# Kernel optimization log

Measured on AMD Instinct MI355X. Metric: run time of the kernel, lower is better.

The kernel has to match this reference:

```python
import jax, jax.numpy as jnp
import numpy as np

V, D, H, L, FF, BS = 50257, 1024, 16, 8, 4096, 1024
B, T = 2, 1024
HD = D // H
SCALE = 1.0 / np.sqrt(HD)
STD = 0.02


def setup_inputs() -> dict:
    key = jax.random.key(0)
    ks = jax.random.split(key, 8)
    rn = lambda k, s: (jax.random.normal(k, s, jnp.float32) * STD)
    return {
        'idx': jax.random.randint(ks[0], (B, T), 0, V),
        'tok_emb': rn(ks[1], (V, D)),
        'pos_emb': rn(ks[2], (1, BS, D)),
        'ln1_w': jnp.ones((L, D)), 'ln1_b': jnp.zeros((L, D)),
        'qkv_w': rn(ks[3], (L, 3 * D, D)), 'qkv_b': jnp.zeros((L, 3 * D)),
        'proj_w': rn(ks[4], (L, D, D)), 'proj_b': jnp.zeros((L, D)),
        'ln2_w': jnp.ones((L, D)), 'ln2_b': jnp.zeros((L, D)),
        'fc1_w': rn(ks[5], (L, FF, D)), 'fc1_b': jnp.zeros((L, FF)),
        'fc2_w': rn(ks[6], (L, D, FF)), 'fc2_b': jnp.zeros((L, D)),
        'lnf_w': jnp.ones((D,)), 'lnf_b': jnp.zeros((D,)),
    }


def layernorm(x, w, b, eps=1e-5):
    mu = jnp.mean(x, axis=-1, keepdims=True)
    var = jnp.mean(jnp.square(x - mu), axis=-1, keepdims=True)
    return (x - mu) * jax.lax.rsqrt(var + eps) * w + b


def _forward(idx, tok_emb, pos_emb, ln1_w, ln1_b, qkv_w, qkv_b, proj_w, proj_b,
             ln2_w, ln2_b, fc1_w, fc1_b, fc2_w, fc2_b, lnf_w, lnf_b):
    b, t = idx.shape
    x = tok_emb[idx] + pos_emb[0, :t]           # [B,T,D]; dropout identity in eval
    mask = jnp.tril(jnp.ones((t, t), dtype=bool))  # causal

    def block(x, p):
        l1w, l1b, qw, qb, pw, pb, l2w, l2b, f1w, f1b, f2w, f2b = p
        h = layernorm(x, l1w, l1b)
        qkv = h @ qw.T + qb                      # [B,T,3D]
        qkv = qkv.reshape(b, t, 3, H, HD)
        q, k, v = qkv[:, :, 0], qkv[:, :, 1], qkv[:, :, 2]  # [B,T,H,HD]
        att = jnp.einsum('bqhd,bkhd->bhqk', q, k) * SCALE
        att = jnp.where(mask, att, -jnp.inf)
        att = jax.nn.softmax(att, axis=-1)       # attn dropout identity in eval
        y = jnp.einsum('bhqk,bkhd->bqhd', att, v).reshape(b, t, D)
        x = x + (y @ pw.T + pb)
        h = layernorm(x, l2w, l2b)
        h = jax.nn.gelu(h @ f1w.T + f1b, approximate=False)  # exact GELU as nn.GELU
        x = x + (h @ f2w.T + f2b)
        return x, None

    params = (ln1_w, ln1_b, qkv_w, qkv_b, proj_w, proj_b,
              ln2_w, ln2_b, fc1_w, fc1_b, fc2_w, fc2_b)
    x, _ = jax.lax.scan(block, x, params)
    x = layernorm(x, lnf_w, lnf_b)
    logits = x @ tok_emb.T                       # weight-tied head
    return logits


def reference(idx, tok_emb, pos_emb, ln1_w, ln1_b, qkv_w, qkv_b, proj_w, proj_b,
              ln2_w, ln2_b, fc1_w, fc1_b, fc2_w, fc2_b, lnf_w, lnf_b):
    return _forward(idx, tok_emb, pos_emb, ln1_w, ln1_b, qkv_w, qkv_b, proj_w,
                    proj_b, ln2_w, ln2_b, fc1_w, fc1_b, fc2_w, fc2_b, lnf_w, lnf_b)
```

## Files before the change

### kernel.cpp

```cpp
#include <hip/hip_runtime.h>
#include <cstdint>

#define Dm 1024
#define Tm 1024
#define Bm 2
#define Lm 8
#define FFm 4096
#define Vm 50257
#define Mm (Bm * Tm)
#define VPAD2 50432

typedef __bf16 bf16x8 __attribute__((ext_vector_type(8)));
typedef float f32x4 __attribute__((ext_vector_type(4)));
typedef unsigned short u16;
typedef unsigned int u32;
typedef u16 u16x8 __attribute__((ext_vector_type(8)));
typedef u16 u16x4 __attribute__((ext_vector_type(4)));

__device__ __forceinline__ u16 f2bf(float f) {
  u32 u = __float_as_uint(f);
  u += 0x7FFFu + ((u >> 16) & 1u);
  return (u16)(u >> 16);
}
__device__ __forceinline__ float bf2f(u16 u) {
  return __uint_as_float((u32)u << 16);
}
__device__ __forceinline__ u32 packbf(float lo, float hi) {
  return (u32)f2bf(lo) | ((u32)f2bf(hi) << 16);
}

__device__ __forceinline__ void gload16(const u16* g, u16* l) {
  __builtin_amdgcn_global_load_lds(
      (const __attribute__((address_space(1))) void*)g,
      (__attribute__((address_space(3))) void*)l, 16, 0, 0);
}

__global__ __launch_bounds__(256) void embed_k(
    const int* __restrict__ idx, const float* __restrict__ tok,
    const float* __restrict__ pos, float* __restrict__ x) {
  int m = blockIdx.x, t = threadIdx.x;
  int id = idx[m];
  int tt = m & (Tm - 1);
  float4 a = *(const float4*)(tok + (size_t)id * Dm + t * 4);
  float4 p = *(const float4*)(pos + (size_t)tt * Dm + t * 4);
  float4 o;
  o.x = a.x + p.x; o.y = a.y + p.y; o.z = a.z + p.z; o.w = a.w + p.w;
  *(float4*)(x + (size_t)m * Dm + t * 4) = o;
}

__global__ __launch_bounds__(256) void conv_k(const float* __restrict__ s,
                                              u16* __restrict__ d,
                                              long long nsrc, long long ntot) {
  long long i = ((long long)blockIdx.x * 256 + threadIdx.x) * 8;
  if (i >= ntot) return;
  u16x8 r = {0, 0, 0, 0, 0, 0, 0, 0};
  if (i < nsrc) {
    float4 a = *(const float4*)(s + i);
    float4 b = *(const float4*)(s + i + 4);
    r[0] = f2bf(a.x); r[1] = f2bf(a.y); r[2] = f2bf(a.z); r[3] = f2bf(a.w);
    r[4] = f2bf(b.x); r[5] = f2bf(b.y); r[6] = f2bf(b.z); r[7] = f2bf(b.w);
  }
  *(u16x8*)(d + i) = r;
}

#define R0 (3 * Dm * Dm)
#define R1 (Dm * Dm)
#define R2 (FFm * Dm)
#define R3 (Dm * FFm)
__global__ __launch_bounds__(256) void convw_k(
    const float* __restrict__ s0, const float* __restrict__ s1,
    const float* __restrict__ s2, const float* __restrict__ s3,
    u16* __restrict__ d) {
  size_t i = ((size_t)blockIdx.x * 256 + threadIdx.x) * 8;
  const float* s;
  size_t o;
  if (i < R0) { s = s0; o = i; }
  else if (i < (size_t)R0 + R1) { s = s1; o = i - R0; }
  else if (i < (size_t)R0 + R1 + R2) { s = s2; o = i - R0 - R1; }
  else { s = s3; o = i - R0 - R1 - R2; }
  float4 a = *(const float4*)(s + o);
  float4 b = *(const float4*)(s + o + 4);
  u16x8 r;
  r[0] = f2bf(a.x); r[1] = f2bf(a.y); r[2] = f2bf(a.z); r[3] = f2bf(a.w);
  r[4] = f2bf(b.x); r[5] = f2bf(b.y); r[6] = f2bf(b.z); r[7] = f2bf(b.w);
  *(u16x8*)(d + i) = r;
}

__global__ __launch_bounds__(256) void ln_k(const float* __restrict__ x,
                                            const float* __restrict__ w,
                                            const float* __restrict__ b,
                                            u16* __restrict__ out) {
  __shared__ float red[4];
  int row = blockIdx.x, t = threadIdx.x;
  float4 v = *(const float4*)(x + (size_t)row * Dm + t * 4);
  float s = v.x + v.y + v.z + v.w;
#pragma unroll
  for (int mm = 1; mm < 64; mm <<= 1) s += __shfl_xor(s, mm);
  if ((t & 63) == 0) red[t >> 6] = s;
  __syncthreads();
  float mu = (red[0] + red[1] + red[2] + red[3]) * (1.0f / Dm);
  __syncthreads();
  float dx = v.x - mu, dy = v.y - mu, dz = v.z - mu, dw = v.w - mu;
  float sq = dx * dx + dy * dy + dz * dz + dw * dw;
#pragma unroll
  for (int mm = 1; mm < 64; mm <<= 1) sq += __shfl_xor(sq, mm);
  if ((t & 63) == 0) red[t >> 6] = sq;
  __syncthreads();
  float var = (red[0] + red[1] + red[2] + red[3]) * (1.0f / Dm);
  float rs = rsqrtf(var + 1e-5f);
  float4 wv = *(const float4*)(w + t * 4);
  float4 bv = *(const float4*)(b + t * 4);
  u16x4 o;
  o[0] = f2bf(dx * rs * wv.x + bv.x);
  o[1] = f2bf(dy * rs * wv.y + bv.y);
  o[2] = f2bf(dz * rs * wv.z + bv.z);
  o[3] = f2bf(dw * rs * wv.w + bv.w);
  *(u16x4*)(out + (size_t)row * Dm + t * 4) = o;
}

__global__ __launch_bounds__(512, 2) void gemm8_k(
    const u16* __restrict__ A, const u16* __restrict__ W,
    const float* __restrict__ bias, float* __restrict__ Cf,
    u16* __restrict__ Cb, int ldc, int nstore, int K, int gelu, int mblks,
    int nblks) {
  __shared__ __align__(16) u16 As[4][8192];
  __shared__ __align__(16) u16 Ws[4][8192];
  int nwg = mblks * nblks;
  int orig = blockIdx.x;
  int q8 = nwg >> 3, r8 = nwg & 7, xcd = orig & 7, loc = orig >> 3;
  int wg = (xcd < r8 ? xcd * (q8 + 1) : r8 * (q8 + 1) + (xcd - r8) * q8) + loc;
  int bx = wg % mblks, by = wg / mblks;
  int m0 = bx << 8, n0 = by << 8;
  int t = threadIdx.x, wave = t >> 6, lane = t & 63;
  int wr = wave >> 2, wc = wave & 3;
  int lr = lane & 15, cq = lane >> 4;
  int sw8 = (cq ^ ((lr >> 1) & 3)) << 3;
  int row0 = t >> 2;
  int kcG = (t & 3) ^ ((t >> 3) & 3);
  const u16* gA = A + (size_t)(m0 + row0) * K + kcG * 8;
  const u16* gW = W + (size_t)(n0 + row0) * K + kcG * 8;
  size_t rstep = (size_t)128 * K;

  f32x4 acc[8][4] = {};
  int nch = K >> 5;

  for (int s = 0; s < 3; ++s) {
    gload16(gA + s * 32, &As[s][wave * 512]);
    gload16(gA + rstep + s * 32, &As[s][4096 + wave * 512]);
    gload16(gW + s * 32, &Ws[s][wave * 512]);
    gload16(gW + rstep + s * 32, &Ws[s][4096 + wave * 512]);
  }
  asm volatile("s_waitcnt vmcnt(8)");
  __builtin_amdgcn_s_barrier();

  for (int c = 0; c < nch; ++c) {
    const u16* sA = As[c & 3];
    const u16* sW = Ws[c & 3];
    bf16x8 afA[4], bfr[4], afB[4];
#pragma unroll
    for (int mi = 0; mi < 4; ++mi)
      afA[mi] = *(const bf16x8*)&sA[(wr * 128 + mi * 16 + lr) * 32 + sw8];
#pragma unroll
    for (int ni = 0; ni < 4; ++ni)
      bfr[ni] = *(const bf16x8*)&sW[(wc * 64 + ni * 16 + lr) * 32 + sw8];
#pragma unroll
    for (int mi = 0; mi < 4; ++mi)
      afB[mi] =
          *(const bf16x8*)&sA[(wr * 128 + (mi + 4) * 16 + lr) * 32 + sw8];
    if (c + 3 < nch) {
      int s3 = (c + 3) & 3;
      gload16(gA + (size_t)(c + 3) * 32, &As[s3][wave * 512]);
      gload16(gA + rstep + (size_t)(c + 3) * 32, &As[s3][4096 + wave * 512]);
    }
    __builtin_amdgcn_s_barrier();
    asm volatile("s_waitcnt lgkmcnt(4)");
    __builtin_amdgcn_s_setprio(1);
#pragma unroll
    for (int mi = 0; mi < 4; ++mi)
#pragma unroll
      for (int ni = 0; ni < 4; ++ni)
        acc[mi][ni] = __builtin_amdgcn_mfma_f32_16x16x32_bf16(
            afA[mi], bfr[ni], acc[mi][ni], 0, 0, 0);
    __builtin_amdgcn_s_setprio(0);
    __builtin_amdgcn_s_barrier();
    if (c + 3 < nch) {
      int s3 = (c + 3) & 3;
      gload16(gW + (size_t)(c + 3) * 32, &Ws[s3][wave * 512]);
      gload16(gW + rstep + (size_t)(c + 3) * 32, &Ws[s3][4096 + wave * 512]);
    }
    asm volatile("s_waitcnt lgkmcnt(0)");
    __builtin_amdgcn_s_setprio(1);
#pragma unroll
    for (int mi = 0; mi < 4; ++mi)
#pragma unroll
      for (int ni = 0; ni < 4; ++ni)
        acc[mi + 4][ni] = __builtin_amdgcn_mfma_f32_16x16x32_bf16(
            afB[mi], bfr[ni], acc[mi + 4][ni], 0, 0, 0);
    __builtin_amdgcn_s_setprio(0);
    if (c + 1 < nch) {
      if (c + 3 < nch)
        asm volatile("s_waitcnt vmcnt(8)");
      else if (c + 2 < nch)
        asm volatile("s_waitcnt vmcnt(4)");
      else
        asm volatile("s_waitcnt vmcnt(0)");
    }
    __builtin_amdgcn_s_barrier();
  }

  int gm0 = m0 + wr * 128 + (cq << 2);
  int gn0 = n0 + wc * 64 + lr;
#pragma unroll
  for (int mi = 0; mi < 8; ++mi) {
#pragma unroll
    for (int ni = 0; ni < 4; ++ni) {
      int gm = gm0 + mi * 16;
      int gn = gn0 + ni * 16;
      if (gn < nstore) {
        float bv = bias ? bias[gn] : 0.f;
#pragma unroll
        for (int j = 0; j < 4; ++j) {
          float o = acc[mi][ni][j] + bv;
          if (gelu) o = 0.5f * o * (1.0f + erff(o * 0.70710678118654752f));
          if (Cb) Cb[(size_t)(gm + j) * ldc + gn] = f2bf(o);
          else Cf[(size_t)(gm + j) * ldc + gn] = o;
        }
      }
    }
  }
}

__global__ __launch_bounds__(512, 2) void gemm8h_k(
    const u16* __restrict__ A, const u16* __restrict__ W,
    const float* __restrict__ bias, float* __restrict__ Cf,
    u16* __restrict__ Cb, int ldc, int nstore, int K, int gelu, int mblks,
    int nblks) {
  __shared__ __align__(16) u16 As[4][4096];
  __shared__ __align__(16) u16 Ws[4][8192];
  int nwg = mblks * nblks;
  int orig = blockIdx.x;
  int q8 = nwg >> 3, r8 = nwg & 7, xcd = orig & 7, loc = orig >> 3;
  int wg = (xcd < r8 ? xcd * (q8 + 1) : r8 * (q8 + 1) + (xcd - r8) * q8) + loc;
  int bx = wg % mblks, by = wg / mblks;
  int m0 = bx << 7, n0 = by << 8;
  int t = threadIdx.x, wave = t >> 6, lane = t & 63;
  int wr = wave >> 2, wc = wave & 3;
  int lr = lane & 15, cq = lane >> 4;
  int sw8 = (cq ^ ((lr >> 1) & 3)) << 3;
  int row0 = t >> 2;
  int kcG = (t & 3) ^ ((t >> 3) & 3);
  const u16* gA = A + (size_t)(m0 + row0) * K + kcG * 8;
  const u16* gW = W + (size_t)(n0 + row0) * K + kcG * 8;
  size_t rstep = (size_t)128 * K;

  f32x4 acc[4][4] = {};
  int nch = K >> 5;

  for (int s = 0; s < 3; ++s) {
    gload16(gA + s * 32, &As[s][wave * 512]);
    gload16(gW + s * 32, &Ws[s][wave * 512]);
    gload16(gW + rstep + s * 32, &Ws[s][4096 + wave * 512]);
  }
  asm volatile("s_waitcnt vmcnt(6)");
  __builtin_amdgcn_s_barrier();

  for (int c = 0; c < nch; ++c) {
    const u16* sA = As[c & 3];
    const u16* sW = Ws[c & 3];
    bf16x8 af[4], bf[4];
#pragma unroll
    for (int mi = 0; mi < 4; ++mi)
      af[mi] = *(const bf16x8*)&sA[(wr * 64 + mi * 16 + lr) * 32 + sw8];
#pragma unroll
    for (int ni = 0; ni < 4; ++ni)
      bf[ni] = *(const bf16x8*)&sW[(wc * 64 + ni * 16 + lr) * 32 + sw8];
    if (c + 3 < nch) {
      int s3 = (c + 3) & 3;
      gload16(gA + (size_t)(c + 3) * 32, &As[s3][wave * 512]);
      gload16(gW + (size_t)(c + 3) * 32, &Ws[s3][wave * 512]);
      gload16(gW + rstep + (size_t)(c + 3) * 32, &Ws[s3][4096 + wave * 512]);
    }
    __builtin_amdgcn_s_barrier();
    asm volatile("s_waitcnt lgkmcnt(0)");
    __builtin_amdgcn_s_setprio(1);
#pragma unroll
    for (int mi = 0; mi < 4; ++mi)
#pragma unroll
      for (int ni = 0; ni < 4; ++ni)
        acc[mi][ni] = __builtin_amdgcn_mfma_f32_16x16x32_bf16(
            af[mi], bf[ni], acc[mi][ni], 0, 0, 0);
    __builtin_amdgcn_s_setprio(0);
    if (c + 1 < nch) {
      if (c + 3 < nch)
        asm volatile("s_waitcnt vmcnt(6)");
      else if (c + 2 < nch)
        asm volatile("s_waitcnt vmcnt(3)");
      else
        asm volatile("s_waitcnt vmcnt(0)");
    }
    __builtin_amdgcn_s_barrier();
  }

  int gm0 = m0 + wr * 64 + (cq << 2);
  int gn0 = n0 + wc * 64 + lr;
#pragma unroll
  for (int mi = 0; mi < 4; ++mi) {
#pragma unroll
    for (int ni = 0; ni < 4; ++ni) {
      int gm = gm0 + mi * 16;
      int gn = gn0 + ni * 16;
      if (gn < nstore) {
        float bv = bias ? bias[gn] : 0.f;
#pragma unroll
        for (int j = 0; j < 4; ++j) {
          float o = acc[mi][ni][j] + bv;
          if (gelu) o = 0.5f * o * (1.0f + erff(o * 0.70710678118654752f));
          if (Cb) Cb[(size_t)(gm + j) * ldc + gn] = f2bf(o);
          else Cf[(size_t)(gm + j) * ldc + gn] = o;
        }
      }
    }
  }
}

__global__ __launch_bounds__(256) void gemm_k(
    const u16* __restrict__ A, const u16* __restrict__ W,
    const float* __restrict__ bias, const float* __restrict__ res,
    float* __restrict__ Cf, u16* __restrict__ Cb, int ldc, int nstore, int K,
    int gelu, int mblks, int nblks) {
  __shared__ __align__(16) u16 As[2][4096];
  __shared__ __align__(16) u16 Ws[2][4096];
  int id = blockIdx.x;
  int c = id & 7, m2 = id >> 3;
  int bx = m2 % mblks;
  int by = (m2 / mblks) * 8 + c;
  if (by >= nblks) return;
  int m0 = bx << 7, n0 = by << 7;
  int t = threadIdx.x;
  int wave = t >> 6, lane = t & 63;
  int wm = (wave & 1) << 6, wn = (wave >> 1) << 6;
  int lr = lane & 15, cq = lane >> 4;

  f32x4 acc[4][4] = {};

  int ch0 = wave * 64 + lane;
  int ch1 = 256 + ch0;
  int r0 = ch0 >> 2, c0 = (ch0 & 3) ^ ((r0 >> 1) & 3);
  int r1 = ch1 >> 2, c1 = (ch1 & 3) ^ ((r1 >> 1) & 3);
  const u16* gA0 = A + (size_t)(m0 + r0) * K + c0 * 8;
  const u16* gA1 = A + (size_t)(m0 + r1) * K + c1 * 8;
  const u16* gW0 = W + (size_t)(n0 + r0) * K + c0 * 8;
  const u16* gW1 = W + (size_t)(n0 + r1) * K + c1 * 8;

  int nst = K >> 5;
  gload16(gA0, &As[0][wave * 512]);
  gload16(gA1, &As[0][2048 + wave * 512]);
  gload16(gW0, &Ws[0][wave * 512]);
  gload16(gW1, &Ws[0][2048 + wave * 512]);
  __syncthreads();

  for (int i = 0; i < nst; ++i) {
    int cur = i & 1;
    if (i + 1 < nst) {
      int ko = (i + 1) << 5;
      gload16(gA0 + ko, &As[cur ^ 1][wave * 512]);
      gload16(gA1 + ko, &As[cur ^ 1][2048 + wave * 512]);
      gload16(gW0 + ko, &Ws[cur ^ 1][wave * 512]);
      gload16(gW1 + ko, &Ws[cur ^ 1][2048 + wave * 512]);
    }
    bf16x8 af[4], bf[4];
#pragma unroll
    for (int mi = 0; mi < 4; ++mi) {
      int rr = wm + mi * 16 + lr;
      af[mi] =
          *(const bf16x8*)&As[cur][rr * 32 + ((cq ^ ((rr >> 1) & 3)) << 3)];
    }
#pragma unroll
    for (int ni = 0; ni < 4; ++ni) {
      int rr = wn + ni * 16 + lr;
      bf[ni] =
          *(const bf16x8*)&Ws[cur][rr * 32 + ((cq ^ ((rr >> 1) & 3)) << 3)];
    }
#pragma unroll
    for (int mi = 0; mi < 4; ++mi)
#pragma unroll
      for (int ni = 0; ni < 4; ++ni)
        acc[mi][ni] = __builtin_amdgcn_mfma_f32_16x16x32_bf16(
            af[mi], bf[ni], acc[mi][ni], 0, 0, 0);
    __syncthreads();
  }

  int orow = cq << 2, ocol = lr;
#pragma unroll
  for (int mi = 0; mi < 4; ++mi) {
#pragma unroll
    for (int ni = 0; ni < 4; ++ni) {
      int gm = m0 + wm + mi * 16 + orow;
      int gn = n0 + wn + ni * 16 + ocol;
      if (gn < nstore) {
        float bv = bias ? bias[gn] : 0.f;
#pragma unroll
        for (int j = 0; j < 4; ++j) {
          float o = acc[mi][ni][j] + bv;
          if (gelu) o = 0.5f * o * (1.0f + erff(o * 0.70710678118654752f));
          if (res) o += res[(size_t)(gm + j) * ldc + gn];
          if (Cb) Cb[(size_t)(gm + j) * ldc + gn] = f2bf(o);
          else Cf[(size_t)(gm + j) * ldc + gn] = o;
        }
      }
    }
  }
}

__global__ __launch_bounds__(256) void gemmsk_k(
    const u16* __restrict__ A, const u16* __restrict__ W,
    const float* __restrict__ bias, float* __restrict__ C, int ldc, int K,
    int klen, int mblks, int nblks) {
  __shared__ __align__(16) u16 As[2][4096];
  __shared__ __align__(16) u16 Ws[2][4096];
  int id = blockIdx.x;
  int bx = id % mblks;
  int tmp = id / mblks;
  int by = tmp % nblks;
  int ks = tmp / nblks;
  int m0 = bx << 7, n0 = by << 7;
  int koff = ks * klen;
  int t = threadIdx.x;
  int wave = t >> 6, lane = t & 63;
  int wm = (wave & 1) << 6, wn = (wave >> 1) << 6;
  int lr = lane & 15, cq = lane >> 4;

  f32x4 acc[4][4] = {};

  int ch0 = wave * 64 + lane;
  int ch1 = 256 + ch0;
  int r0 = ch0 >> 2, c0 = (ch0 & 3) ^ ((r0 >> 1) & 3);
  int r1 = ch1 >> 2, c1 = (ch1 & 3) ^ ((r1 >> 1) & 3);
  const u16* gA0 = A + (size_t)(m0 + r0) * K + koff + c0 * 8;
  const u16* gA1 = A + (size_t)(m0 + r1) * K + koff + c1 * 8;
  const u16* gW0 = W + (size_t)(n0 + r0) * K + koff + c0 * 8;
  const u16* gW1 = W + (size_t)(n0 + r1) * K + koff + c1 * 8;

  int nst = klen >> 5;
  gload16(gA0, &As[0][wave * 512]);
  gload16(gA1, &As[0][2048 + wave * 512]);
  gload16(gW0, &Ws[0][wave * 512]);
  gload16(gW1, &Ws[0][2048 + wave * 512]);
  __syncthreads();

  for (int i = 0; i < nst; ++i) {
    int cur = i & 1;
    if (i + 1 < nst) {
      int ko = (i + 1) << 5;
      gload16(gA0 + ko, &As[cur ^ 1][wave * 512]);
      gload16(gA1 + ko, &As[cur ^ 1][2048 + wave * 512]);
      gload16(gW0 + ko, &Ws[cur ^ 1][wave * 512]);
      gload16(gW1 + ko, &Ws[cur ^ 1][2048 + wave * 512]);
    }
    bf16x8 af[4], bf[4];
#pragma unroll
    for (int mi = 0; mi < 4; ++mi) {
      int rr = wm + mi * 16 + lr;
      af[mi] =
          *(const bf16x8*)&As[cur][rr * 32 + ((cq ^ ((rr >> 1) & 3)) << 3)];
    }
#pragma unroll
    for (int ni = 0; ni < 4; ++ni) {
      int rr = wn + ni * 16 + lr;
      bf[ni] =
          *(const bf16x8*)&Ws[cur][rr * 32 + ((cq ^ ((rr >> 1) & 3)) << 3)];
    }
#pragma unroll
    for (int mi = 0; mi < 4; ++mi)
#pragma unroll
      for (int ni = 0; ni < 4; ++ni)
        acc[mi][ni] = __builtin_amdgcn_mfma_f32_16x16x32_bf16(
            af[mi], bf[ni], acc[mi][ni], 0, 0, 0);
    __syncthreads();
  }

  int orow = cq << 2, ocol = lr;
#pragma unroll
  for (int mi = 0; mi < 4; ++mi) {
#pragma unroll
    for (int ni = 0; ni < 4; ++ni) {
      int gm = m0 + wm + mi * 16 + orow;
      int gn = n0 + wn + ni * 16 + ocol;
      float bv = (ks == 0) ? bias[gn] : 0.f;
#pragma unroll
      for (int j = 0; j < 4; ++j)
        atomicAdd(&C[(size_t)(gm + j) * ldc + gn], acc[mi][ni][j] + bv);
    }
  }
}

__global__ __launch_bounds__(256) void vtr_k(const u16* __restrict__ qkv,
                                             u16* __restrict__ vt) {
  __shared__ u16 T[64 * 68];
  int bh = blockIdx.y;
  int b = bh >> 4, h = bh & 15;
  int t0 = blockIdx.x << 6;
  int tid = threadIdx.x;
  int r = tid >> 2, q4 = tid & 3;
  const u16* src = qkv + (size_t)(b * Tm + t0 + r) * 3072 + 2048 + h * 64 +
                   q4 * 16;
  *(u16x8*)&T[r * 68 + q4 * 16] = *(const u16x8*)src;
  *(u16x8*)&T[r * 68 + q4 * 16 + 8] = *(const u16x8*)(src + 8);
  __syncthreads();
  int dr = tid >> 2, kq = tid & 3;
  u16x8 o0, o1;
#pragma unroll
  for (int u = 0; u < 8; ++u) o0[u] = T[(kq * 16 + u) * 68 + dr];
#pragma unroll
  for (int u = 0; u < 8; ++u) o1[u] = T[(kq * 16 + 8 + u) * 68 + dr];
  u16* dst = vt + ((size_t)bh * 64 + dr) * 1024 + t0 + kq * 16;
  *(u16x8*)dst = o0;
  *(u16x8*)(dst + 8) = o1;
}

__global__ __launch_bounds__(256) void attn_k(const u16* __restrict__ qkv,
                                              const u16* __restrict__ vt,
                                              u16* __restrict__ y) {
  __shared__ __align__(16) u16 Ks[2][4096];
  __shared__ __align__(16) u16 Vs[2][4096];
  int qt = gridDim.x - 1 - blockIdx.x;
  int q0 = qt << 6;
  int bh = blockIdx.y;
  int b = bh >> 4, h = bh & 15;
  int t = threadIdx.x, wave = t >> 6, lane = t & 63;
  int lr = lane & 15, cq = lane >> 4;

  bf16x8 qf[2];
  {
    size_t base = (size_t)(b * Tm + q0 + wave * 16 + lr) * 3072 + h * 64;
#pragma unroll
    for (int ks = 0; ks < 2; ++ks) {
      u16x8 qa = *(const u16x8*)(qkv + base + ks * 32 + cq * 8);
#pragma unroll
      for (int u = 0; u < 8; ++u) qa[u] = f2bf(bf2f(qa[u]) * 0.125f);
      qf[ks] = *(bf16x8*)&qa;
    }
  }

  f32x4 accO[4] = {};
  float m_run = -1e30f, l_run = 0.f;

  int ch0 = wave * 64 + lane, ch1 = 256 + ch0;
  int kr0 = ch0 >> 3, kc0 = ((ch0 & 7) ^ (kr0 & 7)) << 3;
  int kr1 = ch1 >> 3, kc1 = ((ch1 & 7) ^ (kr1 & 7)) << 3;
  const u16* kbase = qkv + (size_t)b * Tm * 3072 + 1024 + h * 64;
  const u16* vbase = vt + (size_t)bh * 64 * 1024;

  {
    gload16(kbase + (size_t)kr0 * 3072 + kc0, &Ks[0][wave * 512]);
    gload16(kbase + (size_t)kr1 * 3072 + kc1, &Ks[0][2048 + wave * 512]);
    gload16(vbase + (size_t)kr0 * 1024 + kc0, &Vs[0][wave * 512]);
    gload16(vbase + (size_t)kr1 * 1024 + kc1, &Vs[0][2048 + wave * 512]);
  }
  __syncthreads();

  for (int tk = 0; tk <= qt; ++tk) {
    int cur = tk & 1;
    if (tk < qt) {
      int kb0 = (tk + 1) << 6;
      gload16(kbase + (size_t)(kb0 + kr0) * 3072 + kc0,
              &Ks[cur ^ 1][wave * 512]);
      gload16(kbase + (size_t)(kb0 + kr1) * 3072 + kc1,
              &Ks[cur ^ 1][2048 + wave * 512]);
      gload16(vbase + (size_t)kr0 * 1024 + kb0 + kc0,
              &Vs[cur ^ 1][wave * 512]);
      gload16(vbase + (size_t)kr1 * 1024 + kb0 + kc1,
              &Vs[cur ^ 1][2048 + wave * 512]);
    }

    f32x4 s[4] = {};
    __builtin_amdgcn_s_setprio(1);
#pragma unroll
    for (int ks = 0; ks < 2; ++ks)
#pragma unroll
      for (int ni = 0; ni < 4; ++ni) {
        int rk = ni * 16 + lr;
        int ck = ks * 4 + cq;
        bf16x8 kf = *(const bf16x8*)&Ks[cur][rk * 64 + ((ck ^ (rk & 7)) << 3)];
        s[ni] = __builtin_amdgcn_mfma_f32_16x16x32_bf16(kf, qf[ks], s[ni],
                                                        0, 0, 0);
      }
    __builtin_amdgcn_s_setprio(0);

    if (tk == qt) {
      int kb0 = tk << 6;
      int qa = q0 + wave * 16 + lr;
#pragma unroll
      for (int ni = 0; ni < 4; ++ni)
#pragma unroll
        for (int r = 0; r < 4; ++r)
          if (kb0 + ni * 16 + cq * 4 + r > qa) s[ni][r] = -1e30f;
    }

    float mx = fmaxf(fmaxf(s[0][0], s[0][1]), fmaxf(s[0][2], s[0][3]));
#pragma unroll
    for (int ni = 1; ni < 4; ++ni)
      mx = fmaxf(mx, fmaxf(fmaxf(s[ni][0], s[ni][1]),
                           fmaxf(s[ni][2], s[ni][3])));
    mx = fmaxf(mx, __shfl_xor(mx, 16));
    mx = fmaxf(mx, __shfl_xor(mx, 32));
    float mn = fmaxf(m_run, mx);
    float alpha = __expf(m_run - mn);
    m_run = mn;
    float ls = 0.f;
    u32 packed[4][2];
#pragma unroll
    for (int ni = 0; ni < 4; ++ni) {
      float p0 = __expf(s[ni][0] - mn), p1 = __expf(s[ni][1] - mn);
      float p2 = __expf(s[ni][2] - mn), p3 = __expf(s[ni][3] - mn);
      ls += (p0 + p1) + (p2 + p3);
      packed[ni][0] = packbf(p0, p1);
      packed[ni][1] = packbf(p2, p3);
    }
    ls += __shfl_xor(ls, 16);
    ls += __shfl_xor(ls, 32);
    l_run = l_run * alpha + ls;

#pragma unroll
    for (int j = 0; j < 4; ++j) {
      float a = __shfl(alpha, (cq << 2) + j);
#pragma unroll
      for (int di = 0; di < 4; ++di) accO[di][j] *= a;
    }

    bf16x8 pf[2];
#pragma unroll
    for (int ks2 = 0; ks2 < 2; ++ks2) {
      union { u32 w[4]; bf16x8 v; } pu;
#pragma unroll
      for (int w = 0; w < 4; ++w) {
        int src = lr + 16 * (((cq & 1) << 1) + (w >> 1));
        int a = __shfl((int)packed[2 * ks2][w & 1], src);
        int bb = __shfl((int)packed[2 * ks2 + 1][w & 1], src);
        pu.w[w] = (cq >> 1) ? (u32)bb : (u32)a;
      }
      pf[ks2] = pu.v;
    }

    __builtin_amdgcn_s_setprio(1);
#pragma unroll
    for (int ks2 = 0; ks2 < 2; ++ks2)
#pragma unroll
      for (int di = 0; di < 4; ++di) {
        int rv = di * 16 + lr;
        int ck = ks2 * 4 + cq;
        bf16x8 vf = *(const bf16x8*)&Vs[cur][rv * 64 + ((ck ^ (rv & 7)) << 3)];
        accO[di] = __builtin_amdgcn_mfma_f32_16x16x32_bf16(pf[ks2], vf,
                                                           accO[di], 0, 0, 0);
      }
    __builtin_amdgcn_s_setprio(0);
    __syncthreads();
  }

  float iv = 1.0f / l_run;
  int qrow = q0 + wave * 16 + (cq << 2);
#pragma unroll
  for (int j = 0; j < 4; ++j) {
    float ivj = __shfl(iv, (cq << 2) + j);
    size_t row = (size_t)(b * Tm + qrow + j) * Dm + h * 64;
#pragma unroll
    for (int di = 0; di < 4; ++di)
      y[row + di * 16 + lr] = f2bf(accO[di][j] * ivj);
  }
}

#define WELEMS ((size_t)(R0 + R1 + R2 + R3))

static inline void launch_gemm(const u16* A, const u16* W, const float* bias,
                               const float* res, float* Cf, u16* Cb, int ldc,
                               int nstore, int K, int gelu, int mblks,
                               int nblks, hipStream_t stream) {
  int gx = 8 * mblks * ((nblks + 7) / 8);
  gemm_k<<<gx, 256, 0, stream>>>(A, W, bias, res, Cf, Cb, ldc, nstore, K,
                                 gelu, mblks, nblks);
}

extern "C" void kernel_launch(void* const* d_in, const int* in_sizes, int n_in,
                              void* d_out, int out_size, void* d_ws,
                              size_t ws_size, hipStream_t stream) {
  const int* idx = (const int*)d_in[0];
  const float* tok = (const float*)d_in[1];
  const float* pos = (const float*)d_in[2];
  const float* ln1w = (const float*)d_in[3];
  const float* ln1b = (const float*)d_in[4];
  const float* qkvw = (const float*)d_in[5];
  const float* qkvb = (const float*)d_in[6];
  const float* projw = (const float*)d_in[7];
  const float* projb = (const float*)d_in[8];
  const float* ln2w = (const float*)d_in[9];
  const float* ln2b = (const float*)d_in[10];
  const float* fc1w = (const float*)d_in[11];
  const float* fc1b = (const float*)d_in[12];
  const float* fc2w = (const float*)d_in[13];
  const float* fc2b = (const float*)d_in[14];
  const float* lnfw = (const float*)d_in[15];
  const float* lnfb = (const float*)d_in[16];
  float* out = (float*)d_out;

  char* w = (char*)d_ws;
  float* x = (float*)w;  w += (size_t)Mm * Dm * 4;
  u16* h = (u16*)w;      w += (size_t)Mm * Dm * 2;
  u16* big = (u16*)w;    w += (size_t)Mm * FFm * 2;
  u16* vtG = (u16*)w;    w += (size_t)Bm * 16 * 64 * Tm * 2;
  u16* wbuf = (u16*)w;   w += WELEMS * 2;
  u16* tokbf = (u16*)w;
  size_t need_full = (size_t)(w - (char*)d_ws) + (size_t)VPAD2 * Dm * 2;
  bool full = ws_size >= need_full;

  embed_k<<<Mm, 256, 0, stream>>>(idx, tok, pos, x);

  if (full) {
    long long nsrc = (long long)Vm * Dm, ntot = (long long)VPAD2 * Dm;
    conv_k<<<(int)((ntot + 2047) / 2048), 256, 0, stream>>>(tok, tokbf, nsrc,
                                                            ntot);
  }

  for (int l = 0; l < Lm; ++l) {
    convw_k<<<(int)(WELEMS / 2048), 256, 0, stream>>>(
        qkvw + (size_t)l * R0, projw + (size_t)l * R1, fc1w + (size_t)l * R2,
        fc2w + (size_t)l * R3, wbuf);
    ln_k<<<Mm, 256, 0, stream>>>(x, ln1w + l * Dm, ln1b + l * Dm, h);
    gemm8h_k<<<(Mm / 128) * ((3 * Dm) / 256), 512, 0, stream>>>(
        h, wbuf, qkvb + (size_t)l * 3 * Dm, nullptr, big, 3 * Dm, 3 * Dm, Dm,
        0, Mm / 128, (3 * Dm) / 256);
    vtr_k<<<dim3(Tm / 64, Bm * 16), 256, 0, stream>>>(big, vtG);
    attn_k<<<dim3(Tm / 64, Bm * 16), 256, 0, stream>>>(big, vtG, h);
    gemmsk_k<<<Mm / 128 * (Dm / 128) * 2, 256, 0, stream>>>(
        h, wbuf + R0, projb + (size_t)l * Dm, x, Dm, Dm, Dm / 2, Mm / 128,
        Dm / 128);
    ln_k<<<Mm, 256, 0, stream>>>(x, ln2w + l * Dm, ln2b + l * Dm, h);
    gemm8h_k<<<(Mm / 128) * (FFm / 256), 512, 0, stream>>>(
        h, wbuf + R0 + R1, fc1b + (size_t)l * FFm, nullptr, big, FFm, FFm,
        Dm, 1, Mm / 128, FFm / 256);
    gemmsk_k<<<Mm / 128 * (Dm / 128) * 4, 256, 0, stream>>>(
        big, wbuf + R0 + R1 + R2, fc2b + (size_t)l * Dm, x, Dm, FFm, FFm / 4,
        Mm / 128, Dm / 128);
  }

  ln_k<<<Mm, 256, 0, stream>>>(x, lnfw, lnfb, h);

  if (full) {
    gemm8_k<<<(Mm / 256) * (VPAD2 / 256), 512, 0, stream>>>(
        h, tokbf, nullptr, out, nullptr, Vm, Vm, Dm, 0, Mm / 256,
        VPAD2 / 256);
  } else {
    for (int c0 = 0; c0 < VPAD2; c0 += 6400) {
      int rows = VPAD2 - c0 < 6400 ? VPAD2 - c0 : 6400;
      long long nsrc = (long long)(Vm - c0 < rows ? (Vm - c0 > 0 ? Vm - c0 : 0)
                                                  : rows) *
                       Dm;
      long long ntot = (long long)rows * Dm;
      conv_k<<<(int)((ntot + 2047) / 2048), 256, 0, stream>>>(
          tok + (size_t)c0 * Dm, wbuf, nsrc, ntot);
      launch_gemm(h, wbuf, nullptr, nullptr, out + c0, nullptr, Vm, Vm - c0,
                  Dm, 0, Mm / 128, rows / 128, stream);
    }
  }
}
```

Baseline: 1.982 ms.

## Make LM head GEMM persistent with cross-tile prefetch and deferred epilogue stores

Replaces the 256x256 one-shot logits GEMM with a persistent kernel launched on 256 workgroups. Each workgroup walks several 128x256 tiles, keeps the global-to-LDS prefetch pipeline running across tile boundaries, and writes the previous tile's fp32 results in batches during the first chunks of the next tile. The intent is to hide the large fp32 logits store and the pipeline fill/drain behind MFMA work, with an XCD-aware tile assignment. In exchange it uses smaller tiles (less data reuse per tile), adds an extra accumulator copy (more register pressure), and relies on hand-tuned vmcnt counts and hardcoded K=1024 and M tiling.

Result: slower. 2.036 ms (+2.7%).

```diff
diff --git a/kernel.cpp b/kernel.cpp
--- a/kernel.cpp
+++ b/kernel.cpp
@@ -34,6 +34,8 @@
       (const __attribute__((address_space(1))) void*)g,
       (__attribute__((address_space(3))) void*)l, 16, 0, 0);
 }
+
+#define WTV(N) asm volatile("s_waitcnt vmcnt(" #N ")")
 
 __global__ __launch_bounds__(256) void embed_k(
     const int* __restrict__ idx, const float* __restrict__ tok,
@@ -118,113 +120,142 @@
   *(u16x4*)(out + (size_t)row * Dm + t * 4) = o;
 }
 
-__global__ __launch_bounds__(512, 2) void gemm8_k(
+__global__ __launch_bounds__(512, 2) void gemm8p_k(
     const u16* __restrict__ A, const u16* __restrict__ W,
-    const float* __restrict__ bias, float* __restrict__ Cf,
-    u16* __restrict__ Cb, int ldc, int nstore, int K, int gelu, int mblks,
-    int nblks) {
-  __shared__ __align__(16) u16 As[4][8192];
+    float* __restrict__ Cf, float* __restrict__ dum, int ldc, int nstore,
+    int nt) {
+  __shared__ __align__(16) u16 As[4][4096];
   __shared__ __align__(16) u16 Ws[4][8192];
-  int nwg = mblks * nblks;
-  int orig = blockIdx.x;
-  int q8 = nwg >> 3, r8 = nwg & 7, xcd = orig & 7, loc = orig >> 3;
-  int wg = (xcd < r8 ? xcd * (q8 + 1) : r8 * (q8 + 1) + (xcd - r8) * q8) + loc;
-  int bx = wg % mblks, by = wg / mblks;
-  int m0 = bx << 8, n0 = by << 8;
+  int bpx = gridDim.x >> 3, npx = nt >> 3;
+  int p = blockIdx.x, xcd = p & 7, kk = p >> 3;
   int t = threadIdx.x, wave = t >> 6, lane = t & 63;
   int wr = wave >> 2, wc = wave & 3;
   int lr = lane & 15, cq = lane >> 4;
   int sw8 = (cq ^ ((lr >> 1) & 3)) << 3;
   int row0 = t >> 2;
   int kcG = (t & 3) ^ ((t >> 3) & 3);
-  const u16* gA = A + (size_t)(m0 + row0) * K + kcG * 8;
-  const u16* gW = W + (size_t)(n0 + row0) * K + kcG * 8;
-  size_t rstep = (size_t)128 * K;
-
-  f32x4 acc[8][4] = {};
-  int nch = K >> 5;
-
-  for (int s = 0; s < 3; ++s) {
-    gload16(gA + s * 32, &As[s][wave * 512]);
-    gload16(gA + rstep + s * 32, &As[s][4096 + wave * 512]);
-    gload16(gW + s * 32, &Ws[s][wave * 512]);
-    gload16(gW + rstep + s * 32, &Ws[s][4096 + wave * 512]);
-  }
-  asm volatile("s_waitcnt vmcnt(8)");
+
+  int ntile = 0;
+  for (int j = kk; j < npx; j += bpx) ++ntile;
+  if (ntile == 0) return;
+  long G = (long)ntile << 5;
+
+  f32x4 acc[4][4] = {};
+  f32x4 sh[4][4];
+  int cgm = 0, cgn = 0, sgm = 0, sgn = 0;
+
+  {
+    int wg0 = npx * xcd + kk;
+    const u16* pA = A + ((size_t)((wg0 & 15) << 7) + row0) * 1024 + kcG * 8;
+    const u16* pW = W + ((size_t)((wg0 >> 4) << 8) + row0) * 1024 + kcG * 8;
+    for (int s = 0; s < 3; ++s) {
+      gload16(pA + s * 32, &As[s][wave * 512]);
+      gload16(pW + s * 32, &Ws[s][wave * 512]);
+      gload16(pW + (size_t)128 * 1024 + s * 32, &Ws[s][4096 + wave * 512]);
+    }
+  }
+  __builtin_amdgcn_sched_barrier(0);
+  WTV(6);
   __builtin_amdgcn_s_barrier();
 
-  for (int c = 0; c < nch; ++c) {
-    const u16* sA = As[c & 3];
-    const u16* sW = Ws[c & 3];
-    bf16x8 afA[4], bfr[4], afB[4];
+  for (long g = 0; g < G; ++g) {
+    int c = (int)(g & 31);
+    int slot = (int)(g & 3);
+    if (c == 0) {
+      if (g) {
+#pragma unroll
+        for (int mi = 0; mi < 4; ++mi)
+#pragma unroll
+          for (int ni = 0; ni < 4; ++ni) {
+            sh[mi][ni] = acc[mi][ni];
+            acc[mi][ni] = (f32x4){0.f, 0.f, 0.f, 0.f};
+          }
+        sgm = cgm;
+        sgn = cgn;
+      }
+      int wg = npx * xcd + kk + bpx * (int)(g >> 5);
+      cgm = ((wg & 15) << 7) + wr * 64 + (cq << 2);
+      cgn = ((wg >> 4) << 8) + wc * 64 + lr;
+    }
+    if (g >= 32 && c < 4) {
+#define SBATCH(MI)                                                        \
+  {                                                                       \
+    _Pragma("unroll") for (int ni = 0; ni < 4; ++ni) {                    \
+      int gn = sgn + ni * 16;                                             \
+      _Pragma("unroll") for (int j = 0; j < 4; ++j) {                     \
+        float* q = (gn < nstore)                                          \
+                       ? (Cf + (size_t)(sgm + MI * 16 + j) * ldc + gn)    \
+                       : (dum + ni * 4 + j);                              \
+        *q = sh[MI][ni][j];                                               \
+      }                                                                   \
+    }                                                                     \
+  }
+      if (c == 0) SBATCH(0)
+      else if (c == 1) SBATCH(1)
+      else if (c == 2) SBATCH(2)
+      else SBATCH(3)
+      __builtin_amdgcn_sched_barrier(0);
+    }
+    const u16* sA = As[slot];
+    const u16* sW = Ws[slot];
+    bf16x8 af[4], bf[4];
 #pragma unroll
     for (int mi = 0; mi < 4; ++mi)
-      afA[mi] = *(const bf16x8*)&sA[(wr * 128 + mi * 16 + lr) * 32 + sw8];
+      af[mi] = *(const bf16x8*)&sA[(wr * 64 + mi * 16 + lr) * 32 + sw8];
 #pragma unroll
     for (int ni = 0; ni < 4; ++ni)
-      bfr[ni] = *(const bf16x8*)&sW[(wc * 64 + ni * 16 + lr) * 32 + sw8];
-#pragma unroll
-    for (int mi = 0; mi < 4; ++mi)
-      afB[mi] =
-          *(const bf16x8*)&sA[(wr * 128 + (mi + 4) * 16 + lr) * 32 + sw8];
-    if (c + 3 < nch) {
-      int s3 = (c + 3) & 3;
-      gload16(gA + (size_t)(c + 3) * 32, &As[s3][wave * 512]);
-      gload16(gA + rstep + (size_t)(c + 3) * 32, &As[s3][4096 + wave * 512]);
+      bf[ni] = *(const bf16x8*)&sW[(wc * 64 + ni * 16 + lr) * 32 + sw8];
+    if (g + 3 < G) {
+      long gg = g + 3;
+      int cc = (int)(gg & 31);
+      int sl = (int)(gg & 3);
+      int wg = npx * xcd + kk + bpx * (int)(gg >> 5);
+      const u16* pA =
+          A + ((size_t)((wg & 15) << 7) + row0) * 1024 + cc * 32 + kcG * 8;
+      const u16* pW =
+          W + ((size_t)((wg >> 4) << 8) + row0) * 1024 + cc * 32 + kcG * 8;
+      gload16(pA, &As[sl][wave * 512]);
+      gload16(pW, &Ws[sl][wave * 512]);
+      gload16(pW + (size_t)128 * 1024, &Ws[sl][4096 + wave * 512]);
     }
     __builtin_amdgcn_s_barrier();
-    asm volatile("s_waitcnt lgkmcnt(4)");
+    asm volatile("s_waitcnt lgkmcnt(0)");
     __builtin_amdgcn_s_setprio(1);
 #pragma unroll
     for (int mi = 0; mi < 4; ++mi)
 #pragma unroll
       for (int ni = 0; ni < 4; ++ni)
         acc[mi][ni] = __builtin_amdgcn_mfma_f32_16x16x32_bf16(
-            afA[mi], bfr[ni], acc[mi][ni], 0, 0, 0);
+            af[mi], bf[ni], acc[mi][ni], 0, 0, 0);
     __builtin_amdgcn_s_setprio(0);
+    if (g + 1 < G) {
+      long r = G - 1 - g;
+      __builtin_amdgcn_sched_barrier(0);
+      if (r < 3) {
+        if (r == 2) WTV(3);
+        else WTV(0);
+      } else if (g >= 32 && c == 0) {
+        WTV(22);
+      } else if (g >= 32 && (c == 1 || c == 2 || c == 3)) {
+        WTV(38);
+      } else if (g >= 32 && c == 4) {
+        WTV(22);
+      } else {
+        WTV(6);
+      }
+    }
     __builtin_amdgcn_s_barrier();
-    if (c + 3 < nch) {
-      int s3 = (c + 3) & 3;
-      gload16(gW + (size_t)(c + 3) * 32, &Ws[s3][wave * 512]);
-      gload16(gW + rstep + (size_t)(c + 3) * 32, &Ws[s3][4096 + wave * 512]);
-    }
-    asm volatile("s_waitcnt lgkmcnt(0)");
-    __builtin_amdgcn_s_setprio(1);
-#pragma unroll
-    for (int mi = 0; mi < 4; ++mi)
-#pragma unroll
-      for (int ni = 0; ni < 4; ++ni)
-        acc[mi + 4][ni] = __builtin_amdgcn_mfma_f32_16x16x32_bf16(
-            afB[mi], bfr[ni], acc[mi + 4][ni], 0, 0, 0);
-    __builtin_amdgcn_s_setprio(0);
-    if (c + 1 < nch) {
-      if (c + 3 < nch)
-        asm volatile("s_waitcnt vmcnt(8)");
-      else if (c + 2 < nch)
-        asm volatile("s_waitcnt vmcnt(4)");
-      else
-        asm volatile("s_waitcnt vmcnt(0)");
-    }
-    __builtin_amdgcn_s_barrier();
-  }
-
-  int gm0 = m0 + wr * 128 + (cq << 2);
-  int gn0 = n0 + wc * 64 + lr;
-#pragma unroll
-  for (int mi = 0; mi < 8; ++mi) {
+  }
+
+#pragma unroll
+  for (int mi = 0; mi < 4; ++mi) {
 #pragma unroll
     for (int ni = 0; ni < 4; ++ni) {
-      int gm = gm0 + mi * 16;
-      int gn = gn0 + ni * 16;
+      int gn = cgn + ni * 16;
       if (gn < nstore) {
-        float bv = bias ? bias[gn] : 0.f;
-#pragma unroll
-        for (int j = 0; j < 4; ++j) {
-          float o = acc[mi][ni][j] + bv;
-          if (gelu) o = 0.5f * o * (1.0f + erff(o * 0.70710678118654752f));
-          if (Cb) Cb[(size_t)(gm + j) * ldc + gn] = f2bf(o);
-          else Cf[(size_t)(gm + j) * ldc + gn] = o;
-        }
+#pragma unroll
+        for (int j = 0; j < 4; ++j)
+          Cf[(size_t)(cgm + mi * 16 + j) * ldc + gn] = acc[mi][ni][j];
       }
     }
   }
@@ -261,7 +292,7 @@
     gload16(gW + s * 32, &Ws[s][wave * 512]);
     gload16(gW + rstep + s * 32, &Ws[s][4096 + wave * 512]);
   }
-  asm volatile("s_waitcnt vmcnt(6)");
+  WTV(6);
   __builtin_amdgcn_s_barrier();
 
   for (int c = 0; c < nch; ++c) {
@@ -292,11 +323,11 @@
     __builtin_amdgcn_s_setprio(0);
     if (c + 1 < nch) {
       if (c + 3 < nch)
-        asm volatile("s_waitcnt vmcnt(6)");
+        WTV(6);
       else if (c + 2 < nch)
-        asm volatile("s_waitcnt vmcnt(3)");
+        WTV(3);
       else
-        asm volatile("s_waitcnt vmcnt(0)");
+        WTV(0);
     }
     __builtin_amdgcn_s_barrier();
   }
@@ -745,9 +776,8 @@
   ln_k<<<Mm, 256, 0, stream>>>(x, lnfw, lnfb, h);
 
   if (full) {
-    gemm8_k<<<(Mm / 256) * (VPAD2 / 256), 512, 0, stream>>>(
-        h, tokbf, nullptr, out, nullptr, Vm, Vm, Dm, 0, Mm / 256,
-        VPAD2 / 256);
+    gemm8p_k<<<256, 512, 0, stream>>>(h, tokbf, out, (float*)big, Vm, Vm,
+                                      (Mm / 128) * (VPAD2 / 256));
   } else {
     for (int c0 = 0; c0 < VPAD2; c0 += 6400) {
       int rows = VPAD2 - c0 < 6400 ? VPAD2 - c0 : 6400;
```
